# Performance work log

Measured on AMD Instinct MI355X. Metric: run time of the kernel, lower is better.

Reference implementation:

```python
import jax, jax.numpy as jnp
import numpy as np

B, S, F, H = 16, 2048, 1024, 16
D = F // H
EPS = 1e-5


def setup_inputs() -> dict:
    key = jax.random.key(0)
    ks = jax.random.split(key, 10)
    scale = 1.0 / np.sqrt(F)
    return {
        "x": jax.random.normal(ks[0], (B, S, F), jnp.float32),
        "Wq": jax.random.normal(ks[1], (F, F), jnp.float32) * scale,
        "bq": jnp.zeros((F,), jnp.float32),
        "Wk": jax.random.normal(ks[2], (F, F), jnp.float32) * scale,
        "bk": jnp.zeros((F,), jnp.float32),
        "Wv": jax.random.normal(ks[3], (F, F), jnp.float32) * scale,
        "bv": jnp.zeros((F,), jnp.float32),
        "Wo": jax.random.normal(ks[4], (F, F), jnp.float32) * scale,
        "bo": jnp.zeros((F,), jnp.float32),
        "gamma": jnp.ones((F,), jnp.float32),
        "beta": jnp.zeros((F,), jnp.float32),
    }


def reference(x, Wq, bq, Wk, bk, Wv, bv, Wo, bo, gamma, beta):
    # x: (B, S, F). Dropout is identity in eval mode.
    b, s, f = x.shape
    q = (x @ Wq + bq).reshape(b, s, H, D)
    k = (x @ Wk + bk).reshape(b, s, H, D)
    v = (x @ Wv + bv).reshape(b, s, H, D)
    # Faithful to source: the einsum (applied to permuted tensors) contracts
    # across HEADS at each sequence position -> scores (B, S, H, H).
    energy = jnp.einsum('bshd,bsgd->bshg', q, k) / (D ** 0.5)
    attn = jax.nn.softmax(energy, axis=-1)  # softmax over key-head axis
    out = jnp.einsum('bshg,bsgd->bshd', attn, v).reshape(b, s, f)
    out = out @ Wo + bo
    # LayerNorm over last dim (eps=1e-5, affine)
    mu = jnp.mean(out, axis=-1, keepdims=True)
    var = jnp.mean((out - mu) ** 2, axis=-1, keepdims=True)
    return (out - mu) * jax.lax.rsqrt(var + EPS) * gamma + beta
```

## Files before the change

### kernel.cpp

```cpp
#include <hip/hip_runtime.h>
#include <hip/hip_bf16.h>
#include <stdint.h>

#define MM   32768
#define FFD  1024
#define NQKV 3072

typedef __bf16 bf16x8 __attribute__((ext_vector_type(8)));
typedef float  f32x4  __attribute__((ext_vector_type(4)));

__device__ __forceinline__ unsigned short f2bf_bits(float f){
  __hip_bfloat16 h = __float2bfloat16(f);
  unsigned short u;
  __builtin_memcpy(&u, &h, 2);
  return u;
}

__device__ __forceinline__ float bf2f(unsigned short u){
  unsigned v = ((unsigned)u) << 16;
  float f;
  __builtin_memcpy(&f, &v, 4);
  return f;
}

__device__ __forceinline__ void gld16(const void* g, void* l){
  const unsigned int* gu = (const unsigned int*)g;
  unsigned int* lu = (unsigned int*)l;
  __builtin_amdgcn_global_load_lds(
      (const __attribute__((address_space(1))) unsigned int*)gu,
      (__attribute__((address_space(3))) unsigned int*)lu,
      16, 0, 0);
}

#define BARRIER() do { asm volatile("" ::: "memory"); \
                       __builtin_amdgcn_s_barrier();  \
                       asm volatile("" ::: "memory"); } while(0)

__global__ __launch_bounds__(256) void k_convert_bf16(const float* __restrict__ in,
                                                      unsigned short* __restrict__ out,
                                                      int n4){
  int i = blockIdx.x * 256 + threadIdx.x;
  if (i >= n4) return;
  float4 v = ((const float4*)in)[i];
  ushort4 r;
  r.x = f2bf_bits(v.x); r.y = f2bf_bits(v.y);
  r.z = f2bf_bits(v.z); r.w = f2bf_bits(v.w);
  ((ushort4*)out)[i] = r;
}

__global__ __launch_bounds__(256) void k_transpose4(const float* __restrict__ Wq,
                                                    const float* __restrict__ Wk,
                                                    const float* __restrict__ Wv,
                                                    const float* __restrict__ Wo,
                                                    unsigned short* __restrict__ Wqkv_t,
                                                    unsigned short* __restrict__ Wo_t){
  __shared__ float tile[32][33];
  const float* in;
  unsigned short* out;
  switch (blockIdx.z){
    case 0:  in = Wq; out = Wqkv_t;               break;
    case 1:  in = Wk; out = Wqkv_t + 1024 * 1024; break;
    case 2:  in = Wv; out = Wqkv_t + 2048 * 1024; break;
    default: in = Wo; out = Wo_t;                 break;
  }
  int bc = blockIdx.x * 32, br = blockIdx.y * 32;
  int tx = threadIdx.x & 31, ty = threadIdx.x >> 5;
  #pragma unroll
  for (int j = 0; j < 32; j += 8)
    tile[ty + j][tx] = in[(size_t)(br + ty + j) * 1024 + bc + tx];
  __syncthreads();
  #pragma unroll
  for (int j = 0; j < 32; j += 8)
    out[(size_t)(bc + ty + j) * 1024 + br + tx] = f2bf_bits(tile[tx][ty + j]);
}

template <bool STATS>
__global__ __launch_bounds__(512, 2) void k_gemm_bt(
    const unsigned short* __restrict__ A,
    const unsigned short* __restrict__ Bt,
    const float* __restrict__ b0, const float* __restrict__ b1, const float* __restrict__ b2,
    unsigned short* __restrict__ Cout, float* __restrict__ stats, int M, int N, int K)
{
  __shared__ alignas(16) char smem[131072];

  const int tid  = threadIdx.x;
  const int lane = tid & 63;
  const int wave = tid >> 6;
  const int wr = wave >> 2, wc = wave & 3;
  const int quad = lane >> 4, lrow = lane & 15;
  const int sa = ((lrow >> 1) & 3) << 4;

  const int nwgx = gridDim.x;
  int nwg = nwgx * gridDim.y;
  int bid = blockIdx.y * nwgx + blockIdx.x;
  int cpx = nwg >> 3;
  int nid = (bid & 7) * cpx + (bid >> 3);
  int by = nid / nwgx;
  int bx = nid - by * nwgx;

  const long rowBase = (long)by * 256;
  const long colBase = (long)bx * 256;

  f32x4 acc[8][4];
  #pragma unroll
  for (int i = 0; i < 8; i++)
    #pragma unroll
    for (int j = 0; j < 4; j++)
      acc[i][j] = (f32x4){0.f, 0.f, 0.f, 0.f};

  const int swz8 = 8 * ((tid & 3) ^ ((tid >> 3) & 3));
  const unsigned short* gA = A  + (rowBase + (tid >> 2)) * (long)K + swz8;
  const unsigned short* gB = Bt + (colBase + (tid >> 2)) * (long)K + swz8;
  const long hstep = 128L * K;

  const int nk = K >> 5;

  #pragma unroll
  for (int tt = 0; tt < 3; ++tt){
    char* nb = smem + tt * 32768;
    gld16(gA + tt * 32,         nb +         tid * 16);
    gld16(gA + tt * 32 + hstep, nb +  8192 + tid * 16);
    gld16(gB + tt * 32,         nb + 16384 + tid * 16);
    gld16(gB + tt * 32 + hstep, nb + 24576 + tid * 16);
  }

  for (int t = 0; t < nk; ++t){
    if (t <= nk - 3)      asm volatile("s_waitcnt vmcnt(8)" ::: "memory");
    else if (t == nk - 2) asm volatile("s_waitcnt vmcnt(4)" ::: "memory");
    else                  asm volatile("s_waitcnt vmcnt(0)" ::: "memory");
    BARRIER();

    char* buf = smem + (t & 3) * 32768;
    if (t < nk - 3){
      char* nb = smem + ((t + 3) & 3) * 32768;
      const unsigned short* sA = gA + (long)(t + 3) * 32;
      const unsigned short* sB = gB + (long)(t + 3) * 32;
      gld16(sA,         nb +         tid * 16);
      gld16(sA + hstep, nb +  8192 + tid * 16);
      gld16(sB,         nb + 16384 + tid * 16);
      gld16(sB + hstep, nb + 24576 + tid * 16);
    }

    bf16x8 bfr[4];
    const char* bb = buf + 16384 + wc * 4096 + lrow * 64 + ((quad * 16) ^ sa);
    #pragma unroll
    for (int n = 0; n < 4; ++n)
      bfr[n] = *(const bf16x8*)(bb + n * 1024);

    #pragma unroll
    for (int p = 0; p < 2; ++p){
      bf16x8 af[4];
      const char* ab = buf + wr * 8192 + p * 4096 + lrow * 64 + ((quad * 16) ^ sa);
      #pragma unroll
      for (int f = 0; f < 4; ++f)
        af[f] = *(const bf16x8*)(ab + f * 1024);
      __builtin_amdgcn_s_setprio(1);
      #pragma unroll
      for (int f = 0; f < 4; ++f)
        #pragma unroll
        for (int n = 0; n < 4; ++n)
          acc[p * 4 + f][n] =
              __builtin_amdgcn_mfma_f32_16x16x32_bf16(af[f], bfr[n], acc[p * 4 + f][n], 0, 0, 0);
      __builtin_amdgcn_s_setprio(0);
    }
  }

  float biasv[4];
  #pragma unroll
  for (int n = 0; n < 4; ++n){
    long col = colBase + wc * 64 + n * 16 + lrow;
    const float* bp = (col < 1024) ? b0 : ((col < 2048) ? b1 : b2);
    biasv[n] = bp[col & 1023];
  }

  if constexpr (STATS){
    #pragma unroll
    for (int m = 0; m < 8; ++m){
      #pragma unroll
      for (int r = 0; r < 4; ++r){
        float p = 0.f, q = 0.f;
        #pragma unroll
        for (int n = 0; n < 4; ++n){
          float v = acc[m][n][r] + biasv[n];
          p += v; q += v * v;
        }
        p += __shfl_xor(p, 1);  q += __shfl_xor(q, 1);
        p += __shfl_xor(p, 2);  q += __shfl_xor(q, 2);
        p += __shfl_xor(p, 4);  q += __shfl_xor(q, 4);
        p += __shfl_xor(p, 8);  q += __shfl_xor(q, 8);
        if (lrow == 0){
          long row = rowBase + wr * 128 + (m >> 2) * 64 + (m & 3) * 16 + quad * 4 + r;
          atomicAdd(&stats[row * 2],     p);
          atomicAdd(&stats[row * 2 + 1], q);
        }
      }
    }
  }

  BARRIER();
  #pragma unroll
  for (int n = 0; n < 4; ++n){
    int lcol = wc * 64 + n * 16 + lrow;
    #pragma unroll
    for (int m = 0; m < 8; ++m){
      int row0 = wr * 128 + (m >> 2) * 64 + (m & 3) * 16 + quad * 4;
      int sw = ((row0 >> 2) & 3) << 5;
      #pragma unroll
      for (int r = 0; r < 4; ++r){
        float v = acc[m][n][r] + biasv[n];
        int byte = (row0 + r) * 512 + ((lcol * 2) ^ sw);
        *(unsigned short*)(smem + byte) = f2bf_bits(v);
      }
    }
  }
  asm volatile("s_waitcnt lgkmcnt(0)" ::: "memory");
  BARRIER();
  #pragma unroll
  for (int i = 0; i < 16; ++i){
    int c = i * 512 + tid;
    int row = c >> 5, cidx = c & 31;
    int rb = (cidx ^ (((row >> 2) & 3) << 1)) * 16;
    uint4 u = *(const uint4*)(smem + row * 512 + rb);
    *(uint4*)(Cout + (rowBase + row) * (long)N + colBase + cidx * 8) = u;
  }
}

__global__ __launch_bounds__(256) void k_attention(const unsigned short* __restrict__ qkv,
                                                   unsigned short* __restrict__ aout){
  const int lane = threadIdx.x & 63;
  const int wave = threadIdx.x >> 6;
  const int pos  = blockIdx.x * 4 + wave;
  const int quad = lane >> 4, lidx = lane & 15;

  const unsigned short* src = qkv + (size_t)pos * 3072;

  f32x4 s = (f32x4){0.f, 0.f, 0.f, 0.f};
  #pragma unroll
  for (int kk = 0; kk < 2; ++kk){
    bf16x8 aK = *(const bf16x8*)(src + 1024 + lidx * 64 + kk * 32 + quad * 8);
    bf16x8 bQ = *(const bf16x8*)(src +        lidx * 64 + kk * 32 + quad * 8);
    s = __builtin_amdgcn_mfma_f32_16x16x32_bf16(aK, bQ, s, 0, 0, 0);
  }

  float v0 = s[0] * 0.125f, v1 = s[1] * 0.125f;
  float v2 = s[2] * 0.125f, v3 = s[3] * 0.125f;
  float m = fmaxf(fmaxf(v0, v1), fmaxf(v2, v3));
  m = fmaxf(m, __shfl_xor(m, 16));
  m = fmaxf(m, __shfl_xor(m, 32));
  float e0 = __expf(v0 - m), e1 = __expf(v1 - m);
  float e2 = __expf(v2 - m), e3 = __expf(v3 - m);
  float sum = e0 + e1 + e2 + e3;
  sum += __shfl_xor(sum, 16);
  sum += __shfl_xor(sum, 32);
  float inv = 1.0f / sum;
  unsigned P01 = (unsigned)f2bf_bits(e0 * inv) | ((unsigned)f2bf_bits(e1 * inv) << 16);
  unsigned P23 = (unsigned)f2bf_bits(e2 * inv) | ((unsigned)f2bf_bits(e3 * inv) << 16);

  int sA = ((quad * 32) + lidx) & 63;
  int sB = (sA + 16) & 63;
  unsigned w0 = (unsigned)__shfl((int)P01, sA);
  unsigned w1 = (unsigned)__shfl((int)P23, sA);
  unsigned w2 = (unsigned)__shfl((int)P01, sB);
  unsigned w3 = (unsigned)__shfl((int)P23, sB);
  if (quad >= 2){ w0 = 0u; w1 = 0u; w2 = 0u; w3 = 0u; }
  union { unsigned u[4]; bf16x8 v; } bp;
  bp.u[0] = w0; bp.u[1] = w1; bp.u[2] = w2; bp.u[3] = w3;

  const unsigned short* Vp = src + 2048;
  unsigned short* dst = aout + (size_t)pos * 1024;
  #pragma unroll
  for (int n4 = 0; n4 < 4; ++n4){
    union { unsigned short us[8]; bf16x8 v; } av;
    #pragma unroll
    for (int j = 0; j < 8; ++j){
      unsigned short rv = Vp[((quad * 8 + j) & 15) * 64 + n4 * 16 + lidx];
      av.us[j] = (quad < 2) ? rv : (unsigned short)0;
    }
    f32x4 o = __builtin_amdgcn_mfma_f32_16x16x32_bf16(
        av.v, bp.v, (f32x4){0.f, 0.f, 0.f, 0.f}, 0, 0, 0);
    unsigned lo = (unsigned)f2bf_bits(o[0]) | ((unsigned)f2bf_bits(o[1]) << 16);
    unsigned hi = (unsigned)f2bf_bits(o[2]) | ((unsigned)f2bf_bits(o[3]) << 16);
    uint2 st; st.x = lo; st.y = hi;
    *(uint2*)(dst + lidx * 64 + n4 * 16 + quad * 4) = st;
  }
}

__global__ __launch_bounds__(256) void k_ln_stats(const unsigned short* __restrict__ ob,
                                                  const float* __restrict__ stats,
                                                  const float* __restrict__ gamma,
                                                  const float* __restrict__ beta,
                                                  float* __restrict__ out){
  int row = blockIdx.x, tid = threadIdx.x;
  float s  = stats[row * 2];
  float ss = stats[row * 2 + 1];
  float mean = s * (1.0f / 1024.0f);
  float var  = ss * (1.0f / 1024.0f) - mean * mean;
  float rstd = rsqrtf(var + 1e-5f);
  ushort4 u = ((const ushort4*)(ob + (size_t)row * 1024))[tid];
  float4 g = ((const float4*)gamma)[tid];
  float4 b = ((const float4*)beta)[tid];
  float4 v;
  v.x = (bf2f(u.x) - mean) * rstd * g.x + b.x;
  v.y = (bf2f(u.y) - mean) * rstd * g.y + b.y;
  v.z = (bf2f(u.z) - mean) * rstd * g.z + b.z;
  v.w = (bf2f(u.w) - mean) * rstd * g.w + b.w;
  ((float4*)(out + (size_t)row * 1024))[tid] = v;
}

extern "C" void kernel_launch(void* const* d_in, const int* in_sizes, int n_in,
                              void* d_out, int out_size, void* d_ws, size_t ws_size,
                              hipStream_t stream){
  const float* x     = (const float*)d_in[0];
  const float* Wq    = (const float*)d_in[1];
  const float* bq    = (const float*)d_in[2];
  const float* Wk    = (const float*)d_in[3];
  const float* bk    = (const float*)d_in[4];
  const float* Wv    = (const float*)d_in[5];
  const float* bv    = (const float*)d_in[6];
  const float* Wo    = (const float*)d_in[7];
  const float* bo    = (const float*)d_in[8];
  const float* gamma = (const float*)d_in[9];
  const float* beta  = (const float*)d_in[10];
  float* out = (float*)d_out;

  char* ws = (char*)d_ws;
  unsigned short* Wqkv_t = (unsigned short*)ws;
  unsigned short* Wo_t   = (unsigned short*)(ws + 6291456);
  unsigned short* xb     = (unsigned short*)(ws + 8388608);
  unsigned short* qkv    = (unsigned short*)(ws + 75497472);
  unsigned short* aout   = xb;
  float*          stats  = (float*)ws;
  unsigned short* obf    = qkv;

  k_convert_bf16<<<32768, 256, 0, stream>>>(x, xb, (MM * FFD) / 4);

  k_transpose4<<<dim3(32, 32, 4), 256, 0, stream>>>(Wq, Wk, Wv, Wo, Wqkv_t, Wo_t);

  k_gemm_bt<false><<<dim3(NQKV / 256, MM / 256), 512, 0, stream>>>(
      xb, Wqkv_t, bq, bk, bv, qkv, nullptr, MM, NQKV, FFD);

  hipMemsetAsync(stats, 0, MM * 2 * sizeof(float), stream);

  k_attention<<<MM / 4, 256, 0, stream>>>(qkv, aout);

  k_gemm_bt<true><<<dim3(FFD / 256, MM / 256), 512, 0, stream>>>(
      aout, Wo_t, bo, bo, bo, obf, stats, MM, FFD, FFD);

  k_ln_stats<<<MM, 256, 0, stream>>>(obf, stats, gamma, beta, out);
}
```

Measured before the change: 673.7 us.

## Shrink GEMM tile to 256x128 with 3-stage pipeline and compute LayerNorm stats in LN kernel

```diff
diff --git a/kernel.cpp b/kernel.cpp
--- a/kernel.cpp
+++ b/kernel.cpp
@@ -74,21 +74,20 @@
     out[(size_t)(bc + ty + j) * 1024 + br + tx] = f2bf_bits(tile[tx][ty + j]);
 }
 
-template <bool STATS>
-__global__ __launch_bounds__(512, 2) void k_gemm_bt(
+__global__ __launch_bounds__(256, 2) void k_gemm_bt(
     const unsigned short* __restrict__ A,
     const unsigned short* __restrict__ Bt,
     const float* __restrict__ b0, const float* __restrict__ b1, const float* __restrict__ b2,
-    unsigned short* __restrict__ Cout, float* __restrict__ stats, int M, int N, int K)
+    unsigned short* __restrict__ Cout, int M, int N, int K)
 {
-  __shared__ alignas(16) char smem[131072];
+  __shared__ alignas(16) char smem[73728];
 
   const int tid  = threadIdx.x;
   const int lane = tid & 63;
   const int wave = tid >> 6;
-  const int wr = wave >> 2, wc = wave & 3;
+  const int wr = wave >> 1, wc = wave & 1;
   const int quad = lane >> 4, lrow = lane & 15;
-  const int sa = ((lrow >> 1) & 3) << 4;
+  const int csw = ((quad ^ (lrow & 3)) << 4);
 
   const int nwgx = gridDim.x;
   int nwg = nwgx * gridDim.y;
@@ -99,7 +98,7 @@
   int bx = nid - by * nwgx;
 
   const long rowBase = (long)by * 256;
-  const long colBase = (long)bx * 256;
+  const long colBase = (long)bx * 128;
 
   f32x4 acc[8][4];
   #pragma unroll
@@ -108,41 +107,39 @@
     for (int j = 0; j < 4; j++)
       acc[i][j] = (f32x4){0.f, 0.f, 0.f, 0.f};
 
-  const int swz8 = 8 * ((tid & 3) ^ ((tid >> 3) & 3));
+  const int swz8 = 8 * ((tid & 3) ^ ((tid >> 2) & 3));
   const unsigned short* gA = A  + (rowBase + (tid >> 2)) * (long)K + swz8;
   const unsigned short* gB = Bt + (colBase + (tid >> 2)) * (long)K + swz8;
-  const long hstep = 128L * K;
+  const long r64 = 64L * K;
+  const int t16 = tid * 16;
 
   const int nk = K >> 5;
 
-  #pragma unroll
-  for (int tt = 0; tt < 3; ++tt){
-    char* nb = smem + tt * 32768;
-    gld16(gA + tt * 32,         nb +         tid * 16);
-    gld16(gA + tt * 32 + hstep, nb +  8192 + tid * 16);
-    gld16(gB + tt * 32,         nb + 16384 + tid * 16);
-    gld16(gB + tt * 32 + hstep, nb + 24576 + tid * 16);
-  }
+  auto STAGE = [&](int u, int s){
+    char* base = smem + s * 24576;
+    const unsigned short* a = gA + (long)u * 32;
+    const unsigned short* b = gB + (long)u * 32;
+    gld16(a,           base +         t16);
+    gld16(a + r64,     base +  4096 + t16);
+    gld16(a + 2 * r64, base +  8192 + t16);
+    gld16(a + 3 * r64, base + 12288 + t16);
+    gld16(b,           base + 16384 + t16);
+    gld16(b + r64,     base + 20480 + t16);
+  };
+
+  STAGE(0, 0);
+  STAGE(1, 1);
 
   for (int t = 0; t < nk; ++t){
-    if (t <= nk - 3)      asm volatile("s_waitcnt vmcnt(8)" ::: "memory");
-    else if (t == nk - 2) asm volatile("s_waitcnt vmcnt(4)" ::: "memory");
-    else                  asm volatile("s_waitcnt vmcnt(0)" ::: "memory");
+    if (t < nk - 1) asm volatile("s_waitcnt vmcnt(6)" ::: "memory");
+    else            asm volatile("s_waitcnt vmcnt(0)" ::: "memory");
     BARRIER();
 
-    char* buf = smem + (t & 3) * 32768;
-    if (t < nk - 3){
-      char* nb = smem + ((t + 3) & 3) * 32768;
-      const unsigned short* sA = gA + (long)(t + 3) * 32;
-      const unsigned short* sB = gB + (long)(t + 3) * 32;
-      gld16(sA,         nb +         tid * 16);
-      gld16(sA + hstep, nb +  8192 + tid * 16);
-      gld16(sB,         nb + 16384 + tid * 16);
-      gld16(sB + hstep, nb + 24576 + tid * 16);
-    }
+    char* buf = smem + (t % 3) * 24576;
+    if (t < nk - 2) STAGE(t + 2, (t + 2) % 3);
 
     bf16x8 bfr[4];
-    const char* bb = buf + 16384 + wc * 4096 + lrow * 64 + ((quad * 16) ^ sa);
+    const char* bb = buf + 16384 + wc * 4096 + lrow * 64 + csw;
     #pragma unroll
     for (int n = 0; n < 4; ++n)
       bfr[n] = *(const bf16x8*)(bb + n * 1024);
@@ -150,7 +147,7 @@
     #pragma unroll
     for (int p = 0; p < 2; ++p){
       bf16x8 af[4];
-      const char* ab = buf + wr * 8192 + p * 4096 + lrow * 64 + ((quad * 16) ^ sa);
+      const char* ab = buf + wr * 8192 + p * 4096 + lrow * 64 + csw;
       #pragma unroll
       for (int f = 0; f < 4; ++f)
         af[f] = *(const bf16x8*)(ab + f * 1024);
@@ -165,50 +162,20 @@
     }
   }
 
-  float biasv[4];
+  BARRIER();
   #pragma unroll
   for (int n = 0; n < 4; ++n){
-    long col = colBase + wc * 64 + n * 16 + lrow;
+    int lcol = wc * 64 + n * 16 + lrow;
+    long col = colBase + lcol;
     const float* bp = (col < 1024) ? b0 : ((col < 2048) ? b1 : b2);
-    biasv[n] = bp[col & 1023];
-  }
-
-  if constexpr (STATS){
+    float bias = bp[col & 1023];
     #pragma unroll
     for (int m = 0; m < 8; ++m){
+      int row0 = wr * 128 + (m >> 2) * 64 + (m & 3) * 16 + quad * 4;
       #pragma unroll
       for (int r = 0; r < 4; ++r){
-        float p = 0.f, q = 0.f;
-        #pragma unroll
-        for (int n = 0; n < 4; ++n){
-          float v = acc[m][n][r] + biasv[n];
-          p += v; q += v * v;
-        }
-        p += __shfl_xor(p, 1);  q += __shfl_xor(q, 1);
-        p += __shfl_xor(p, 2);  q += __shfl_xor(q, 2);
-        p += __shfl_xor(p, 4);  q += __shfl_xor(q, 4);
-        p += __shfl_xor(p, 8);  q += __shfl_xor(q, 8);
-        if (lrow == 0){
-          long row = rowBase + wr * 128 + (m >> 2) * 64 + (m & 3) * 16 + quad * 4 + r;
-          atomicAdd(&stats[row * 2],     p);
-          atomicAdd(&stats[row * 2 + 1], q);
-        }
-      }
-    }
-  }
-
-  BARRIER();
-  #pragma unroll
-  for (int n = 0; n < 4; ++n){
-    int lcol = wc * 64 + n * 16 + lrow;
-    #pragma unroll
-    for (int m = 0; m < 8; ++m){
-      int row0 = wr * 128 + (m >> 2) * 64 + (m & 3) * 16 + quad * 4;
-      int sw = ((row0 >> 2) & 3) << 5;
-      #pragma unroll
-      for (int r = 0; r < 4; ++r){
-        float v = acc[m][n][r] + biasv[n];
-        int byte = (row0 + r) * 512 + ((lcol * 2) ^ sw);
+        float v = acc[m][n][r] + bias;
+        int byte = (row0 + r) * 256 + ((lcol * 2) ^ (quad << 5));
         *(unsigned short*)(smem + byte) = f2bf_bits(v);
       }
     }
@@ -217,10 +184,10 @@
   BARRIER();
   #pragma unroll
   for (int i = 0; i < 16; ++i){
-    int c = i * 512 + tid;
-    int row = c >> 5, cidx = c & 31;
+    int c = i * 256 + tid;
+    int row = c >> 4, cidx = c & 15;
     int rb = (cidx ^ (((row >> 2) & 3) << 1)) * 16;
-    uint4 u = *(const uint4*)(smem + row * 512 + rb);
+    uint4 u = *(const uint4*)(smem + row * 256 + rb);
     *(uint4*)(Cout + (rowBase + row) * (long)N + colBase + cidx * 8) = u;
   }
 }
@@ -285,25 +252,36 @@
   }
 }
 
-__global__ __launch_bounds__(256) void k_ln_stats(const unsigned short* __restrict__ ob,
-                                                  const float* __restrict__ stats,
-                                                  const float* __restrict__ gamma,
-                                                  const float* __restrict__ beta,
-                                                  float* __restrict__ out){
-  int row = blockIdx.x, tid = threadIdx.x;
-  float s  = stats[row * 2];
-  float ss = stats[row * 2 + 1];
-  float mean = s * (1.0f / 1024.0f);
-  float var  = ss * (1.0f / 1024.0f) - mean * mean;
+__global__ __launch_bounds__(256) void k_ln_bf16(const unsigned short* __restrict__ ob,
+                                                 const float* __restrict__ gamma,
+                                                 const float* __restrict__ beta,
+                                                 float* __restrict__ out){
+  __shared__ float red[8];
+  int tid = threadIdx.x;
+  int row = blockIdx.x;
+  ushort4 u = ((const ushort4*)(ob + (size_t)row * 1024))[tid];
+  float x0 = bf2f(u.x), x1 = bf2f(u.y), x2 = bf2f(u.z), x3 = bf2f(u.w);
+  float s  = x0 + x1 + x2 + x3;
+  float ss = x0 * x0 + x1 * x1 + x2 * x2 + x3 * x3;
+  #pragma unroll
+  for (int off = 32; off > 0; off >>= 1){
+    s  += __shfl_down(s, off);
+    ss += __shfl_down(ss, off);
+  }
+  if ((tid & 63) == 0){ red[tid >> 6] = s; red[4 + (tid >> 6)] = ss; }
+  __syncthreads();
+  float S  = red[0] + red[1] + red[2] + red[3];
+  float SS = red[4] + red[5] + red[6] + red[7];
+  float mean = S * (1.0f / 1024.0f);
+  float var  = SS * (1.0f / 1024.0f) - mean * mean;
   float rstd = rsqrtf(var + 1e-5f);
-  ushort4 u = ((const ushort4*)(ob + (size_t)row * 1024))[tid];
   float4 g = ((const float4*)gamma)[tid];
   float4 b = ((const float4*)beta)[tid];
   float4 v;
-  v.x = (bf2f(u.x) - mean) * rstd * g.x + b.x;
-  v.y = (bf2f(u.y) - mean) * rstd * g.y + b.y;
-  v.z = (bf2f(u.z) - mean) * rstd * g.z + b.z;
-  v.w = (bf2f(u.w) - mean) * rstd * g.w + b.w;
+  v.x = (x0 - mean) * rstd * g.x + b.x;
+  v.y = (x1 - mean) * rstd * g.y + b.y;
+  v.z = (x2 - mean) * rstd * g.z + b.z;
+  v.w = (x3 - mean) * rstd * g.w + b.w;
   ((float4*)(out + (size_t)row * 1024))[tid] = v;
 }
 
@@ -329,22 +307,19 @@
   unsigned short* xb     = (unsigned short*)(ws + 8388608);
   unsigned short* qkv    = (unsigned short*)(ws + 75497472);
   unsigned short* aout   = xb;
-  float*          stats  = (float*)ws;
   unsigned short* obf    = qkv;
 
   k_convert_bf16<<<32768, 256, 0, stream>>>(x, xb, (MM * FFD) / 4);
 
   k_transpose4<<<dim3(32, 32, 4), 256, 0, stream>>>(Wq, Wk, Wv, Wo, Wqkv_t, Wo_t);
 
-  k_gemm_bt<false><<<dim3(NQKV / 256, MM / 256), 512, 0, stream>>>(
-      xb, Wqkv_t, bq, bk, bv, qkv, nullptr, MM, NQKV, FFD);
-
-  hipMemsetAsync(stats, 0, MM * 2 * sizeof(float), stream);
+  k_gemm_bt<<<dim3(NQKV / 128, MM / 256), 256, 0, stream>>>(
+      xb, Wqkv_t, bq, bk, bv, qkv, MM, NQKV, FFD);
 
   k_attention<<<MM / 4, 256, 0, stream>>>(qkv, aout);
 
-  k_gemm_bt<true><<<dim3(FFD / 256, MM / 256), 512, 0, stream>>>(
-      aout, Wo_t, bo, bo, bo, obf, stats, MM, FFD, FFD);
-
-  k_ln_stats<<<MM, 256, 0, stream>>>(obf, stats, gamma, beta, out);
-}
+  k_gemm_bt<<<dim3(FFD / 128, MM / 256), 256, 0, stream>>>(
+      aout, Wo_t, bo, bo, bo, obf, MM, FFD, FFD);
+
+  k_ln_bf16<<<MM, 256, 0, stream>>>(obf, gamma, beta, out);
+}
```

Result: faster. 626.6 us (-7.0%).

## Fuse output projection GEMM with LayerNorm using full-row tiles

Applied to the files above, without the earlier changes.

```diff
diff --git a/kernel.cpp b/kernel.cpp
--- a/kernel.cpp
+++ b/kernel.cpp
@@ -14,13 +14,6 @@
   unsigned short u;
   __builtin_memcpy(&u, &h, 2);
   return u;
-}
-
-__device__ __forceinline__ float bf2f(unsigned short u){
-  unsigned v = ((unsigned)u) << 16;
-  float f;
-  __builtin_memcpy(&f, &v, 4);
-  return f;
 }
 
 __device__ __forceinline__ void gld16(const void* g, void* l){
@@ -74,12 +67,11 @@
     out[(size_t)(bc + ty + j) * 1024 + br + tx] = f2bf_bits(tile[tx][ty + j]);
 }
 
-template <bool STATS>
 __global__ __launch_bounds__(512, 2) void k_gemm_bt(
     const unsigned short* __restrict__ A,
     const unsigned short* __restrict__ Bt,
     const float* __restrict__ b0, const float* __restrict__ b1, const float* __restrict__ b2,
-    unsigned short* __restrict__ Cout, float* __restrict__ stats, int M, int N, int K)
+    unsigned short* __restrict__ Cout, int M, int N, int K)
 {
   __shared__ alignas(16) char smem[131072];
 
@@ -165,49 +157,20 @@
     }
   }
 
-  float biasv[4];
-  #pragma unroll
-  for (int n = 0; n < 4; ++n){
-    long col = colBase + wc * 64 + n * 16 + lrow;
-    const float* bp = (col < 1024) ? b0 : ((col < 2048) ? b1 : b2);
-    biasv[n] = bp[col & 1023];
-  }
-
-  if constexpr (STATS){
-    #pragma unroll
-    for (int m = 0; m < 8; ++m){
-      #pragma unroll
-      for (int r = 0; r < 4; ++r){
-        float p = 0.f, q = 0.f;
-        #pragma unroll
-        for (int n = 0; n < 4; ++n){
-          float v = acc[m][n][r] + biasv[n];
-          p += v; q += v * v;
-        }
-        p += __shfl_xor(p, 1);  q += __shfl_xor(q, 1);
-        p += __shfl_xor(p, 2);  q += __shfl_xor(q, 2);
-        p += __shfl_xor(p, 4);  q += __shfl_xor(q, 4);
-        p += __shfl_xor(p, 8);  q += __shfl_xor(q, 8);
-        if (lrow == 0){
-          long row = rowBase + wr * 128 + (m >> 2) * 64 + (m & 3) * 16 + quad * 4 + r;
-          atomicAdd(&stats[row * 2],     p);
-          atomicAdd(&stats[row * 2 + 1], q);
-        }
-      }
-    }
-  }
-
   BARRIER();
   #pragma unroll
   for (int n = 0; n < 4; ++n){
     int lcol = wc * 64 + n * 16 + lrow;
+    long col = colBase + lcol;
+    const float* bp = (col < 1024) ? b0 : ((col < 2048) ? b1 : b2);
+    float bias = bp[col & 1023];
     #pragma unroll
     for (int m = 0; m < 8; ++m){
       int row0 = wr * 128 + (m >> 2) * 64 + (m & 3) * 16 + quad * 4;
       int sw = ((row0 >> 2) & 3) << 5;
       #pragma unroll
       for (int r = 0; r < 4; ++r){
-        float v = acc[m][n][r] + biasv[n];
+        float v = acc[m][n][r] + bias;
         int byte = (row0 + r) * 512 + ((lcol * 2) ^ sw);
         *(unsigned short*)(smem + byte) = f2bf_bits(v);
       }
@@ -222,6 +185,148 @@
     int rb = (cidx ^ (((row >> 2) & 3) << 1)) * 16;
     uint4 u = *(const uint4*)(smem + row * 512 + rb);
     *(uint4*)(Cout + (rowBase + row) * (long)N + colBase + cidx * 8) = u;
+  }
+}
+
+__global__ __launch_bounds__(512) void k_gemm2_ln(
+    const unsigned short* __restrict__ A,
+    const unsigned short* __restrict__ Bt,
+    const float* __restrict__ bo,
+    const float* __restrict__ gamma, const float* __restrict__ beta,
+    float* __restrict__ out)
+{
+  __shared__ alignas(16) char smem[69632];
+
+  const int tid  = threadIdx.x;
+  const int lane = tid & 63;
+  const int wave = tid >> 6;
+  const int quad = lane >> 4, lrow = lane & 15;
+  const int csw  = (quad ^ ((lrow >> 1) & 3)) << 4;
+
+  int nwg = gridDim.x;
+  int bid = blockIdx.x;
+  int cpx = nwg >> 3;
+  int nid = (bid & 7) * cpx + (bid >> 3);
+  const long rowBase = (long)nid * 64;
+
+  f32x4 acc[4][8];
+  #pragma unroll
+  for (int i = 0; i < 4; i++)
+    #pragma unroll
+    for (int j = 0; j < 8; j++)
+      acc[i][j] = (f32x4){0.f, 0.f, 0.f, 0.f};
+
+  const int swz8 = 8 * ((tid & 3) ^ ((tid >> 3) & 3));
+  const unsigned short* gA = A + (rowBase + (tid >> 2)) * 1024L + swz8;
+  const int t16 = tid * 16;
+  const int nk = 32;
+
+  if (tid < 256){
+    gld16(gA,      smem        + t16);
+    gld16(gA + 32, smem + 4096 + t16);
+  }
+
+  for (int t = 0; t < nk; ++t){
+    if (t < nk - 1) asm volatile("s_waitcnt vmcnt(1)" ::: "memory");
+    else            asm volatile("s_waitcnt vmcnt(0)" ::: "memory");
+    BARRIER();
+
+    const char* buf = smem + (t % 3) * 4096;
+
+    bf16x8 bfr[8];
+    #pragma unroll
+    for (int n = 0; n < 8; ++n)
+      bfr[n] = *(const bf16x8*)(Bt + (size_t)(wave * 128 + n * 16 + lrow) * 1024 + t * 32 + quad * 8);
+    bf16x8 af[4];
+    #pragma unroll
+    for (int m = 0; m < 4; ++m)
+      af[m] = *(const bf16x8*)(buf + (m * 16 + lrow) * 64 + csw);
+
+    if (t < nk - 2 && tid < 256)
+      gld16(gA + (long)(t + 2) * 32, smem + ((t + 2) % 3) * 4096 + t16);
+
+    __builtin_amdgcn_s_setprio(1);
+    #pragma unroll
+    for (int m = 0; m < 4; ++m)
+      #pragma unroll
+      for (int n = 0; n < 8; ++n)
+        acc[m][n] = __builtin_amdgcn_mfma_f32_16x16x32_bf16(af[m], bfr[n], acc[m][n], 0, 0, 0);
+    __builtin_amdgcn_s_setprio(0);
+  }
+
+  float gv[8], bv[8];
+  #pragma unroll
+  for (int n = 0; n < 8; ++n){
+    int col = wave * 128 + n * 16 + lrow;
+    float bias = bo[col];
+    gv[n] = gamma[col]; bv[n] = beta[col];
+    #pragma unroll
+    for (int m = 0; m < 4; ++m)
+      #pragma unroll
+      for (int r = 0; r < 4; ++r)
+        acc[m][n][r] += bias;
+  }
+
+  float* stats = (float*)(smem + 65536);
+  #pragma unroll
+  for (int m = 0; m < 4; ++m)
+    #pragma unroll
+    for (int r = 0; r < 4; ++r){
+      float p = 0.f, q = 0.f;
+      #pragma unroll
+      for (int n = 0; n < 8; ++n){
+        float v = acc[m][n][r];
+        p += v; q += v * v;
+      }
+      p += __shfl_xor(p, 1);  q += __shfl_xor(q, 1);
+      p += __shfl_xor(p, 2);  q += __shfl_xor(q, 2);
+      p += __shfl_xor(p, 4);  q += __shfl_xor(q, 4);
+      p += __shfl_xor(p, 8);  q += __shfl_xor(q, 8);
+      if (lrow == 0){
+        int row = m * 16 + quad * 4 + r;
+        stats[(wave * 64 + row) * 2]     = p;
+        stats[(wave * 64 + row) * 2 + 1] = q;
+      }
+    }
+  asm volatile("s_waitcnt lgkmcnt(0)" ::: "memory");
+  BARRIER();
+
+  #pragma unroll
+  for (int m = 0; m < 4; ++m){
+    float meanr[4], rstdr[4];
+    #pragma unroll
+    for (int r = 0; r < 4; ++r){
+      int row = m * 16 + quad * 4 + r;
+      float S = 0.f, SS = 0.f;
+      #pragma unroll
+      for (int w = 0; w < 8; ++w){
+        S  += stats[(w * 64 + row) * 2];
+        SS += stats[(w * 64 + row) * 2 + 1];
+      }
+      float mean = S * (1.0f / 1024.0f);
+      float var  = SS * (1.0f / 1024.0f) - mean * mean;
+      meanr[r] = mean;
+      rstdr[r] = rsqrtf(var + 1e-5f);
+    }
+    #pragma unroll
+    for (int n = 0; n < 8; ++n){
+      int col = wave * 128 + n * 16 + lrow;
+      #pragma unroll
+      for (int r = 0; r < 4; ++r){
+        float v = (acc[m][n][r] - meanr[r]) * rstdr[r] * gv[n] + bv[n];
+        *(float*)(smem + (quad * 4 + r) * 4096 + col * 4) = v;
+      }
+    }
+    asm volatile("s_waitcnt lgkmcnt(0)" ::: "memory");
+    BARRIER();
+    #pragma unroll
+    for (int i = 0; i < 8; ++i){
+      int c = i * 512 + tid;
+      int row = c >> 8, cx = c & 255;
+      uint4 u = *(const uint4*)(smem + row * 4096 + cx * 16);
+      *(uint4*)(out + (rowBase + m * 16 + row) * 1024 + cx * 4) = u;
+    }
+    BARRIER();
   }
 }
 
@@ -283,28 +388,6 @@
     uint2 st; st.x = lo; st.y = hi;
     *(uint2*)(dst + lidx * 64 + n4 * 16 + quad * 4) = st;
   }
-}
-
-__global__ __launch_bounds__(256) void k_ln_stats(const unsigned short* __restrict__ ob,
-                                                  const float* __restrict__ stats,
-                                                  const float* __restrict__ gamma,
-                                                  const float* __restrict__ beta,
-                                                  float* __restrict__ out){
-  int row = blockIdx.x, tid = threadIdx.x;
-  float s  = stats[row * 2];
-  float ss = stats[row * 2 + 1];
-  float mean = s * (1.0f / 1024.0f);
-  float var  = ss * (1.0f / 1024.0f) - mean * mean;
-  float rstd = rsqrtf(var + 1e-5f);
-  ushort4 u = ((const ushort4*)(ob + (size_t)row * 1024))[tid];
-  float4 g = ((const float4*)gamma)[tid];
-  float4 b = ((const float4*)beta)[tid];
-  float4 v;
-  v.x = (bf2f(u.x) - mean) * rstd * g.x + b.x;
-  v.y = (bf2f(u.y) - mean) * rstd * g.y + b.y;
-  v.z = (bf2f(u.z) - mean) * rstd * g.z + b.z;
-  v.w = (bf2f(u.w) - mean) * rstd * g.w + b.w;
-  ((float4*)(out + (size_t)row * 1024))[tid] = v;
 }
 
 extern "C" void kernel_launch(void* const* d_in, const int* in_sizes, int n_in,
@@ -329,22 +412,15 @@
   unsigned short* xb     = (unsigned short*)(ws + 8388608);
   unsigned short* qkv    = (unsigned short*)(ws + 75497472);
   unsigned short* aout   = xb;
-  float*          stats  = (float*)ws;
-  unsigned short* obf    = qkv;
 
   k_convert_bf16<<<32768, 256, 0, stream>>>(x, xb, (MM * FFD) / 4);
 
   k_transpose4<<<dim3(32, 32, 4), 256, 0, stream>>>(Wq, Wk, Wv, Wo, Wqkv_t, Wo_t);
 
-  k_gemm_bt<false><<<dim3(NQKV / 256, MM / 256), 512, 0, stream>>>(
-      xb, Wqkv_t, bq, bk, bv, qkv, nullptr, MM, NQKV, FFD);
-
-  hipMemsetAsync(stats, 0, MM * 2 * sizeof(float), stream);
+  k_gemm_bt<<<dim3(NQKV / 256, MM / 256), 512, 0, stream>>>(
+      xb, Wqkv_t, bq, bk, bv, qkv, MM, NQKV, FFD);
 
   k_attention<<<MM / 4, 256, 0, stream>>>(qkv, aout);
 
-  k_gemm_bt<true><<<dim3(FFD / 256, MM / 256), 512, 0, stream>>>(
-      aout, Wo_t, bo, bo, bo, obf, stats, MM, FFD, FFD);
-
-  k_ln_stats<<<MM, 256, 0, stream>>>(obf, stats, gamma, beta, out);
-}
+  k_gemm2_ln<<<MM / 64, 512, 0, stream>>>(aout, Wo_t, bo, gamma, beta, out);
+}
```

New measurement: 697.4 us. +3.5%, slower.
